# Kernel optimization log

Hardware: AMD Instinct MI355X
Metric: run time of the kernel (lower is better)

The kernel has to match this reference:

```python
import jax, jax.numpy as jnp
import numpy as np

NUM_GROUPS = 32
EPS = 1e-6
NUM_HEADS = 8


def group_norm32(x, gamma, beta):
    # GroupNorm32: compute in float32, cast back to input dtype.
    b, c, h, w = x.shape
    xf = x.astype(jnp.float32).reshape(b, NUM_GROUPS, -1)  # [b, G, (C/G)*h*w]
    mean = xf.mean(axis=-1, keepdims=True)
    var = xf.var(axis=-1, keepdims=True)
    xn = ((xf - mean) * jax.lax.rsqrt(var + EPS)).reshape(b, c, h, w)
    xn = xn * gamma[None, :, None, None] + beta[None, :, None, None]
    return xn.astype(x.dtype)


def setup_inputs() -> dict:
    key = jax.random.key(0)
    ks = jax.random.split(key, 4)
    b, c, h, w = 16, 512, 32, 32
    x = jax.random.normal(ks[0], (b, c, h, w), dtype=jnp.float32)
    w_qkv = jax.random.normal(ks[1], (3 * c, c), dtype=jnp.float32) * (1.0 / np.sqrt(c))
    b_qkv = jnp.zeros((3 * c,), dtype=jnp.float32)
    w_proj = jax.random.normal(ks[2], (c, c), dtype=jnp.float32) * (1.0 / np.sqrt(c))
    b_proj = jnp.zeros((c,), dtype=jnp.float32)
    gamma = jnp.ones((c,), dtype=jnp.float32)
    beta = jnp.zeros((c,), dtype=jnp.float32)
    return {"x": x, "w_qkv": w_qkv, "b_qkv": b_qkv, "w_proj": w_proj,
            "b_proj": b_proj, "gamma": gamma, "beta": beta}


def reference(x, w_qkv, b_qkv, w_proj, b_proj, gamma, beta):
    b, c, h, w = x.shape
    H = NUM_HEADS
    d = c // H
    n = h * w
    x_norm = group_norm32(x, gamma, beta)
    # 1x1 conv == channel matmul
    qkv = jnp.einsum('oc,bchw->bohw', w_qkv, x_norm) + b_qkv[None, :, None, None]
    q, k, v = jnp.split(qkv, 3, axis=1)
    q = q.reshape(b, H, d, n)
    k = k.reshape(b, H, d, n)
    v = v.reshape(b, H, d, n)
    scale = d ** (-0.5)
    attn = jnp.einsum('bhdn,bhdm->bhnm', q, k) * scale  # [b,H,n,n]
    attn = jax.nn.softmax(attn, axis=-1)
    out = jnp.einsum('bhnm,bhdm->bhdn', attn, v).reshape(b, c, h, w)
    proj = jnp.einsum('oc,bchw->bohw', w_proj, out) + b_proj[None, :, None, None]
    return x + proj
```

## Files before the change

### kernel.cpp

```cpp
#include <hip/hip_runtime.h>
#include <hip/hip_bf16.h>

typedef __bf16 bf16;
typedef __bf16 bf16x4 __attribute__((ext_vector_type(4)));
typedef __bf16 bf16x8 __attribute__((ext_vector_type(8)));
typedef float  floatx4 __attribute__((ext_vector_type(4)));
typedef float  f32x16  __attribute__((ext_vector_type(16)));

#define BB   16
#define CC   512
#define NN   1024
#define GG   32
#define CPG  16
#define HH   8
#define DD   64
#define QSCALE 0.18033688011f

#if __has_builtin(__builtin_amdgcn_exp2f)
#define EXP2(x) __builtin_amdgcn_exp2f(x)
#else
#define EXP2(x) exp2f(x)
#endif

__device__ inline floatx4 mfma16(bf16x8 a, bf16x8 b, floatx4 c) {
    return __builtin_amdgcn_mfma_f32_16x16x32_bf16(a, b, c, 0, 0, 0);
}
__device__ inline f32x16 mfma32(bf16x8 a, bf16x8 b, f32x16 c) {
    return __builtin_amdgcn_mfma_f32_32x32x16_bf16(a, b, c, 0, 0, 0);
}

__device__ inline floatx4 zero4() {
    floatx4 z; z[0] = 0.f; z[1] = 0.f; z[2] = 0.f; z[3] = 0.f; return z;
}

__device__ inline void gl_lds16(const bf16* g, bf16* l) {
    __builtin_amdgcn_global_load_lds(
        (const __attribute__((address_space(1))) unsigned int*)g,
        (__attribute__((address_space(3))) unsigned int*)l, 16, 0, 0);
}

__device__ inline unsigned cvt_pk_bf16(float a, float b) {
    unsigned r;
    asm("v_cvt_pk_bf16_f32 %0, %1, %2" : "=v"(r) : "v"(a), "v"(b));
    return r;
}
__device__ inline void pl32swap(unsigned &x, unsigned &y) {
    asm volatile("v_permlane32_swap_b32 %0, %1" : "+v"(x), "+v"(y));
}

__device__ inline float ldf(const void* p, size_t i, int isb) {
    return isb ? (float)((const bf16*)p)[i] : ((const float*)p)[i];
}
__device__ inline floatx4 ldf4(const void* p, size_t i, int isb) {
    floatx4 o;
    if (isb) {
        bf16x4 v = *(const bf16x4*)((const bf16*)p + i);
        #pragma unroll
        for (int j = 0; j < 4; ++j) o[j] = (float)v[j];
    } else {
        o = *(const floatx4*)((const float*)p + i);
    }
    return o;
}
__device__ inline void stf(void* p, size_t i, float v, int isb) {
    if (isb) ((bf16*)p)[i] = (bf16)v; else ((float*)p)[i] = v;
}

__global__ __launch_bounds__(256) void flag_kernel(const void* x, const void* wq,
        const void* wp, const void* gamma, int* flags) {
    __shared__ int bad[3];
    const int tid = threadIdx.x;
    if (tid < 3) bad[tid] = 0;
    __syncthreads();
    const void* arrs[3] = {x, wq, wp};
    #pragma unroll
    for (int a = 0; a < 3; ++a) {
        const unsigned short* u = (const unsigned short*)arrs[a];
        int c = 0;
        for (int i = tid * 32; i < tid * 32 + 32; ++i) {
            if ((u[i] & 0x7F80) == 0x7F80) c = 1;
        }
        if (c) atomicOr(&bad[a], 1);
    }
    __syncthreads();
    if (tid == 0) {
        flags[0] = bad[0] ? 0 : 1;
        flags[1] = bad[1] ? 0 : 1;
        flags[2] = bad[2] ? 0 : 1;
        flags[3] = (((const unsigned short*)gamma)[0] == 0x3F80) ? 1 : 0;
    }
}

__global__ __launch_bounds__(256) void cvt2_kernel(const void* __restrict__ src1,
        const void* __restrict__ src2, bf16* __restrict__ dst1,
        bf16* __restrict__ dst2, const int* __restrict__ flags) {
    const int NQKV = 3 * CC * CC;
    int i = (blockIdx.x * 256 + threadIdx.x) * 4;
    const void* src; bf16* dst; int f;
    if (i < NQKV) {
        src = src1; dst = dst1; f = flags[1];
    } else {
        src = src2; dst = dst2; f = flags[2]; i -= NQKV;
    }
    if (f) {
        *(bf16x4*)(dst + i) = *(const bf16x4*)((const bf16*)src + i);
    } else {
        const float* s = (const float*)src + i;
        bf16x4 o;
        #pragma unroll
        for (int j = 0; j < 4; ++j) o[j] = (bf16)s[j];
        *(bf16x4*)(dst + i) = o;
    }
}

__global__ __launch_bounds__(256) void gn_kernel(const void* __restrict__ x,
        const void* __restrict__ gamma, const void* __restrict__ beta,
        bf16* __restrict__ xn_t, const int* __restrict__ flags, int b0) {
    const int fx = flags[0], fg = flags[3];
    const int bg = blockIdx.x;
    const int bl = bg >> 5, g = bg & 31;
    const int tid = threadIdx.x;
    const size_t xbase = (size_t)((b0 + bl) * CC + g * CPG) * NN;

    float s = 0.f, ss = 0.f;
    for (int i = tid * 4; i < CPG * NN; i += 1024) {
        floatx4 v = ldf4(x, xbase + i, fx);
        #pragma unroll
        for (int j = 0; j < 4; ++j) { s += v[j]; ss += v[j] * v[j]; }
    }
    for (int off = 32; off > 0; off >>= 1) {
        s  += __shfl_down(s, off);
        ss += __shfl_down(ss, off);
    }
    __shared__ float red[8];
    __shared__ float stats[2];
    const int wave = tid >> 6;
    if ((tid & 63) == 0) { red[wave] = s; red[4 + wave] = ss; }
    __syncthreads();
    if (tid == 0) {
        float S  = red[0] + red[1] + red[2] + red[3];
        float SS = red[4] + red[5] + red[6] + red[7];
        float mean = S * (1.0f / (CPG * NN));
        float var  = SS * (1.0f / (CPG * NN)) - mean * mean;
        stats[0] = mean;
        stats[1] = rsqrtf(fmaxf(var, 0.f) + 1e-6f);
    }
    __syncthreads();
    const float mean = stats[0], rstd = stats[1];

    __shared__ __align__(16) float tile[4][CPG][66];
    const int l = tid & 63;
    const int cn = l >> 2;
    const int nb = (l & 3) * 16;
    const float gm1 = ldf(gamma, g * CPG + cn, fg);
    const float bt1 = ldf(beta,  g * CPG + cn, fg);
    const int n2 = l >> 2, cq = l & 3;
    float (*tw)[66] = tile[wave];

    for (int nt = wave; nt < NN / 64; nt += 4) {
        #pragma unroll
        for (int k = 0; k < 4; ++k) {
            floatx4 v = ldf4(x, xbase + (size_t)cn * NN + nt * 64 + nb + k * 4, fx);
            #pragma unroll
            for (int j = 0; j < 4; ++j)
                tw[cn][nb + k * 4 + j] = (v[j] - mean) * rstd * gm1 + bt1;
        }
        asm volatile("s_waitcnt lgkmcnt(0)" ::: "memory");
        #pragma unroll
        for (int m = 0; m < 4; ++m) {
            const int n2m = n2 + m * 16;
            bf16x4 o;
            #pragma unroll
            for (int k = 0; k < 4; ++k) o[k] = (bf16)tw[cq * 4 + k][n2m];
            *(bf16x4*)(xn_t + (size_t)(bl * NN + nt * 64 + n2m) * CC + g * CPG + cq * 4) = o;
        }
        asm volatile("s_waitcnt lgkmcnt(0)" ::: "memory");
    }
}

__global__ __launch_bounds__(256) void qkv_kernel(const bf16* __restrict__ wq_b,
        const bf16* __restrict__ b_qkv, const bf16* __restrict__ xn_t,
        bf16* __restrict__ q_t, bf16* __restrict__ k_pk, bf16* __restrict__ v_pk) {
    __shared__ __align__(16) bf16 As[2][128 * 32];
    __shared__ __align__(16) bf16 Bs[2][128 * 32];

    const int ntile = blockIdx.x;
    const int mtile = blockIdx.y;
    const int bl = blockIdx.z;
    const int w = threadIdx.x >> 6, lane = threadIdx.x & 63;
    const int l16 = lane & 15, quad = lane >> 4;
    const int wr = w >> 1, wc = w & 1;

    const int mbase = mtile * 128, nbase = ntile * 128;
    const int srow = lane >> 2;
    const int scol = (((lane & 3) ^ ((srow >> 1) & 3)) << 3);
    const bf16* Ag = wq_b + (size_t)(mbase + w * 32 + srow) * CC + scol;
    const bf16* Bg = xn_t + (size_t)bl * NN * CC + (size_t)(nbase + w * 32 + srow) * CC + scol;
    const int ldso = (2 * w) * 512;

#define QSTAGE(buf, k0) do {                                  \
    gl_lds16(Ag + (k0),           &As[buf][ldso]);            \
    gl_lds16(Ag + 16 * CC + (k0), &As[buf][ldso + 512]);      \
    gl_lds16(Bg + (k0),           &Bs[buf][ldso]);            \
    gl_lds16(Bg + 16 * CC + (k0), &Bs[buf][ldso + 512]);      \
} while (0)

    floatx4 acc[4][4];
    #pragma unroll
    for (int i = 0; i < 4; ++i)
        #pragma unroll
        for (int j = 0; j < 4; ++j) acc[i][j] = zero4();

    const int sw = (l16 >> 1) & 3;
    QSTAGE(0, 0);

    for (int it = 0; it < 16; ++it) {
        const int cur = it & 1;
        const int nk = ((it + 1) & 15) * 32;
        QSTAGE(cur ^ 1, nk);
        asm volatile("s_waitcnt vmcnt(4)" ::: "memory");
        __builtin_amdgcn_s_barrier();

        bf16x8 af[4], bfr[4];
        #pragma unroll
        for (int mt = 0; mt < 4; ++mt)
            af[mt] = *(const bf16x8*)&As[cur][(wr * 64 + mt * 16 + l16) * 32 + ((quad ^ sw) << 3)];
        #pragma unroll
        for (int nt = 0; nt < 4; ++nt)
            bfr[nt] = *(const bf16x8*)&Bs[cur][(wc * 64 + nt * 16 + l16) * 32 + ((quad ^ sw) << 3)];

        asm volatile("s_waitcnt lgkmcnt(0)" ::: "memory");
        __builtin_amdgcn_s_barrier();

        #pragma unroll
        for (int mt = 0; mt < 4; ++mt)
            #pragma unroll
            for (int nt = 0; nt < 4; ++nt)
                acc[mt][nt] = mfma16(af[mt], bfr[nt], acc[mt][nt]);
    }
#undef QSTAGE

    const int qsel = mtile >> 2;
    const int obase = (mtile & 3) * 128;
    #pragma unroll
    for (int mt = 0; mt < 4; ++mt) {
        const int op = obase + wr * 64 + mt * 16 + quad * 4;
        float bias[4];
        #pragma unroll
        for (int r = 0; r < 4; ++r) bias[r] = (float)b_qkv[qsel * CC + op + r];
        #pragma unroll
        for (int nt = 0; nt < 4; ++nt) {
            const int p = nbase + wc * 64 + nt * 16 + l16;
            if (qsel == 0) {
                int h = op >> 6, d0 = op & 63;
                bf16x4 o;
                #pragma unroll
                for (int r = 0; r < 4; ++r) o[r] = (bf16)((acc[mt][nt][r] + bias[r]) * QSCALE);
                *(bf16x4*)(q_t + ((size_t)(bl * HH + h) * NN + p) * DD + d0) = o;
            } else if (qsel == 1) {
                int h = op >> 6, d0 = op & 63;
                bf16x4 o;
                #pragma unroll
                for (int r = 0; r < 4; ++r) o[r] = (bf16)(acc[mt][nt][r] + bias[r]);
                size_t off = ((size_t)(bl * HH + h) << 16) + ((size_t)(p >> 5) << 11)
                           + ((d0 >> 4) << 9) + (((d0 >> 3) & 1) << 8)
                           + ((p & 31) << 3) + (d0 & 7);
                *(bf16x4*)(k_pk + off) = o;
            } else {
                #pragma unroll
                for (int r = 0; r < 4; ++r) {
                    int c = op + r;
                    int h = c >> 6, d = c & 63;
                    size_t off = ((size_t)(bl * HH + h) << 16) + ((size_t)(p >> 4) << 10)
                               + ((d >> 5) << 9) + (((p >> 3) & 1) << 8)
                               + ((d & 31) << 3) + (p & 7);
                    v_pk[off] = (bf16)(acc[mt][nt][r] + bias[r]);
                }
            }
        }
    }
}

__global__ __launch_bounds__(256) void attn_kernel(const bf16* __restrict__ q_t,
        const bf16* __restrict__ k_pk, const bf16* __restrict__ v_pk,
        bf16* __restrict__ attn_out) {
    const int lid = blockIdx.x + (blockIdx.y << 2);
    const int xcd = lid & 7, jj = lid >> 3;
    const int bh = xcd * (gridDim.y >> 3) + (jj >> 2);
    const int qb = jj & 3;
    const int bl = bh >> 3, h = bh & 7;
    const int tid = threadIdx.x;
    const int w = tid >> 6, lane = tid & 63;
    const int l31 = lane & 31, hi = lane >> 5;

    const bf16* kpb = k_pk + ((size_t)bh << 16) + (hi << 8) + (l31 << 3);
    const bf16* vpb = v_pk + ((size_t)bh << 16) + (hi << 8) + (l31 << 3);

    const int qbase = qb * 256 + w * 64;
    const bf16* qp = q_t + ((size_t)bh * NN + qbase + l31) * DD + hi * 8;
    bf16x8 qf0[4], qf1[4];
    #pragma unroll
    for (int ks = 0; ks < 4; ++ks) {
        qf0[ks] = *(const bf16x8*)(qp + ks * 16);
        qf1[ks] = *(const bf16x8*)(qp + (size_t)32 * DD + ks * 16);
    }

    f32x16 oacc0[2], oacc1[2];
    #pragma unroll
    for (int i = 0; i < 2; ++i)
        #pragma unroll
        for (int r = 0; r < 16; ++r) { oacc0[i][r] = 0.f; oacc1[i][r] = 0.f; }
    float lrun0 = 0.f, lrun1 = 0.f;

#define EXPPACK(SV, PW, LR) do {                                          \
    float p[16];                                                          \
    _Pragma("unroll")                                                     \
    for (int r = 0; r < 16; ++r) { p[r] = EXP2((SV)[r]); LR += p[r]; }    \
    _Pragma("unroll")                                                     \
    for (int i = 0; i < 8; ++i) PW[i] = cvt_pk_bf16(p[2*i], p[2*i+1]);    \
    pl32swap(PW[0], PW[2]); pl32swap(PW[1], PW[3]);                       \
    pl32swap(PW[4], PW[6]); pl32swap(PW[5], PW[7]);                       \
} while (0)

    bf16x8 kf[4];
    #pragma unroll
    for (int ks = 0; ks < 4; ++ks)
        kf[ks] = *(const bf16x8*)(kpb + (ks << 9));

    #pragma unroll 2
    for (int kb = 0; kb < 32; ++kb) {
        bf16x8 vfr[4];
        #pragma unroll
        for (int tt = 0; tt < 2; ++tt)
            #pragma unroll
            for (int db = 0; db < 2; ++db)
                vfr[tt * 2 + db] = *(const bf16x8*)(vpb + (size_t)((kb * 2 + tt) << 10) + (db << 9));
        const int kbn = (kb + 1) & 31;
        bf16x8 kfn[4];
        #pragma unroll
        for (int ks = 0; ks < 4; ++ks)
            kfn[ks] = *(const bf16x8*)(kpb + (size_t)(kbn << 11) + (ks << 9));

        f32x16 s0, s1;
        #pragma unroll
        for (int r = 0; r < 16; ++r) { s0[r] = 0.f; s1[r] = 0.f; }
        #pragma unroll
        for (int ks = 0; ks < 4; ++ks) s0 = mfma32(kf[ks], qf0[ks], s0);
        #pragma unroll
        for (int ks = 0; ks < 4; ++ks) s1 = mfma32(kf[ks], qf1[ks], s1);

        unsigned pw0[8], pw1[8];
        EXPPACK(s0, pw0, lrun0);
        EXPPACK(s1, pw1, lrun1);

        #pragma unroll
        for (int tt = 0; tt < 2; ++tt) {
            union { unsigned u[4]; bf16x8 v; } pf0, pf1;
            #pragma unroll
            for (int i = 0; i < 4; ++i) {
                pf0.u[i] = pw0[tt * 4 + i];
                pf1.u[i] = pw1[tt * 4 + i];
            }
            #pragma unroll
            for (int db = 0; db < 2; ++db) {
                bf16x8 vf = vfr[tt * 2 + db];
                oacc0[db] = mfma32(vf, pf0.v, oacc0[db]);
                oacc1[db] = mfma32(vf, pf1.v, oacc1[db]);
            }
        }
        #pragma unroll
        for (int ks = 0; ks < 4; ++ks) kf[ks] = kfn[ks];
    }
#undef EXPPACK

    lrun0 += __shfl_xor(lrun0, 32);
    lrun1 += __shfl_xor(lrun1, 32);
    const float inv0 = 1.0f / lrun0;
    const float inv1 = 1.0f / lrun1;
    bf16* ob0 = attn_out + ((size_t)bl * NN + qbase + l31) * CC + h * DD;
    bf16* ob1 = ob0 + (size_t)32 * CC;
    #pragma unroll
    for (int db = 0; db < 2; ++db) {
        #pragma unroll
        for (int g = 0; g < 4; ++g) {
            bf16x4 o0, o1;
            #pragma unroll
            for (int e = 0; e < 4; ++e) {
                o0[e] = (bf16)(oacc0[db][4 * g + e] * inv0);
                o1[e] = (bf16)(oacc1[db][4 * g + e] * inv1);
            }
            *(bf16x4*)(ob0 + db * 32 + g * 8 + hi * 4) = o0;
            *(bf16x4*)(ob1 + db * 32 + g * 8 + hi * 4) = o1;
        }
    }
}

__global__ __launch_bounds__(256) void proj_kernel(const bf16* __restrict__ wp_b,
        const bf16* __restrict__ b_proj, const bf16* __restrict__ attn_out,
        const void* __restrict__ x, void* __restrict__ out,
        const int* __restrict__ flags, int b0) {
    __shared__ __align__(16) bf16 As[2][128 * 32];
    __shared__ __align__(16) bf16 Bs[2][128 * 32];

    const int fx = flags[0];
    const int ntile = blockIdx.x;
    const int mtile = blockIdx.y;
    const int bl = blockIdx.z;
    const int w = threadIdx.x >> 6, lane = threadIdx.x & 63;
    const int l16 = lane & 15, quad = lane >> 4;
    const int wr = w >> 1, wc = w & 1;

    const int mbase = mtile * 128, nbase = ntile * 128;
    const int srow = lane >> 2;
    const int scol = (((lane & 3) ^ ((srow >> 1) & 3)) << 3);
    const bf16* Ag = wp_b + (size_t)(mbase + w * 32 + srow) * CC + scol;
    const bf16* Bg = attn_out + (size_t)bl * NN * CC + (size_t)(nbase + w * 32 + srow) * CC + scol;
    const int ldso = (2 * w) * 512;

#define PSTAGE(buf, k0) do {                                  \
    gl_lds16(Ag + (k0),           &As[buf][ldso]);            \
    gl_lds16(Ag + 16 * CC + (k0), &As[buf][ldso + 512]);      \
    gl_lds16(Bg + (k0),           &Bs[buf][ldso]);            \
    gl_lds16(Bg + 16 * CC + (k0), &Bs[buf][ldso + 512]);      \
} while (0)

    floatx4 acc[4][4];
    #pragma unroll
    for (int i = 0; i < 4; ++i)
        #pragma unroll
        for (int j = 0; j < 4; ++j) acc[i][j] = zero4();

    const int sw = (l16 >> 1) & 3;
    PSTAGE(0, 0);

    for (int it = 0; it < 16; ++it) {
        const int cur = it & 1;
        const int nk = ((it + 1) & 15) * 32;
        PSTAGE(cur ^ 1, nk);
        asm volatile("s_waitcnt vmcnt(4)" ::: "memory");
        __builtin_amdgcn_s_barrier();

        bf16x8 af[4], bfr[4];
        #pragma unroll
        for (int mt = 0; mt < 4; ++mt)
            af[mt] = *(const bf16x8*)&As[cur][(wr * 64 + mt * 16 + l16) * 32 + ((quad ^ sw) << 3)];
        #pragma unroll
        for (int nt = 0; nt < 4; ++nt)
            bfr[nt] = *(const bf16x8*)&Bs[cur][(wc * 64 + nt * 16 + l16) * 32 + ((quad ^ sw) << 3)];

        asm volatile("s_waitcnt lgkmcnt(0)" ::: "memory");
        __builtin_amdgcn_s_barrier();

        #pragma unroll
        for (int mt = 0; mt < 4; ++mt)
            #pragma unroll
            for (int nt = 0; nt < 4; ++nt)
                acc[mt][nt] = mfma16(af[mt], bfr[nt], acc[mt][nt]);
    }
#undef PSTAGE

    #pragma unroll
    for (int mt = 0; mt < 4; ++mt) {
        const int op = mbase + wr * 64 + mt * 16 + quad * 4;
        float bias[4];
        #pragma unroll
        for (int r = 0; r < 4; ++r) bias[r] = (float)b_proj[op + r];
        #pragma unroll
        for (int nt = 0; nt < 4; ++nt) {
            const int p = nbase + wc * 64 + nt * 16 + l16;
            #pragma unroll
            for (int r = 0; r < 4; ++r) {
                size_t idx = ((size_t)(b0 + bl) * CC + op + r) * NN + p;
                float xv = ldf(x, idx, fx);
                stf(out, idx, xv + acc[mt][nt][r] + bias[r], fx);
            }
        }
    }
}

extern "C" void kernel_launch(void* const* d_in, const int* in_sizes, int n_in,
                              void* d_out, int out_size, void* d_ws, size_t ws_size,
                              hipStream_t stream) {
    const void* x      = d_in[0];
    const void* w_qkv  = d_in[1];
    const bf16* b_qkv  = (const bf16*)d_in[2];
    const void* w_proj = d_in[3];
    const bf16* b_proj = (const bf16*)d_in[4];
    const void* gamma  = d_in[5];
    const void* beta   = d_in[6];

    const size_t MB = (size_t)1 << 20;
    const int NQKV = 3 * CC * CC;
    const int NPRJ = CC * CC;
    const size_t wbytes = (size_t)(NQKV + NPRJ) * sizeof(bf16) + 4096;
    int bc = 0;
    for (int c = 16; c >= 1; c >>= 1) {
        if ((size_t)c * 4 * MB + wbytes <= ws_size) { bc = c; break; }
    }
    if (bc == 0) {
        hipMemsetAsync(d_out, 0, (size_t)out_size * sizeof(bf16), stream);
        return;
    }

    const size_t cs = (size_t)bc * MB;
    char* ws = (char*)d_ws;
    bf16* xn_t = (bf16*)(ws);
    bf16* q_t  = (bf16*)(ws + cs);
    bf16* k_pk = (bf16*)(ws + 2 * cs);
    bf16* v_pk = (bf16*)(ws + 3 * cs);
    int*  flags = (int*)(ws + 4 * cs);
    bf16* wq_b = (bf16*)(ws + 4 * cs + 4096);
    bf16* wp_b = wq_b + NQKV;
    bf16* attn_out = xn_t;

    flag_kernel<<<1, 256, 0, stream>>>(x, w_qkv, w_proj, gamma, flags);
    cvt2_kernel<<<(NQKV + NPRJ) / 1024, 256, 0, stream>>>(w_qkv, w_proj, wq_b, wp_b, flags);

    for (int b0 = 0; b0 < BB; b0 += bc) {
        gn_kernel<<<dim3(bc * GG), 256, 0, stream>>>(x, gamma, beta, xn_t, flags, b0);
        qkv_kernel<<<dim3(8, 12, bc), 256, 0, stream>>>(wq_b, b_qkv, xn_t, q_t, k_pk, v_pk);
        attn_kernel<<<dim3(4, bc * HH), 256, 0, stream>>>(q_t, k_pk, v_pk, attn_out);
        proj_kernel<<<dim3(8, 4, bc), 256, 0, stream>>>(wp_b, b_proj, attn_out, x, d_out, flags, b0);
    }
}
```

Baseline: 231.3 us.

## Enlarge QKV GEMM tiles to 256x256x64 with 8 waves and staged prefetch

Reworks the QKV projection GEMM so each 512-thread block computes a 256x256 output tile with K-steps of 64, where previously 256-thread blocks computed 128x128 tiles with K-steps of 32. Global-to-LDS prefetch of the next stage is split into four quarters interleaved with the MFMA sub-phases, and s_setprio raises wave priority around the MFMA bursts. The aim is more operand reuse per LDS load and fewer barriers per FLOP. In exchange the grid shrinks to 24 blocks per batch, LDS use grows to 128 KB per block, and register pressure rises, which may lower occupancy and leave CUs underused at small batch chunks.

```diff
diff --git a/kernel.cpp b/kernel.cpp
--- a/kernel.cpp
+++ b/kernel.cpp
@@ -178,103 +178,155 @@
     }
 }
 
-__global__ __launch_bounds__(256) void qkv_kernel(const bf16* __restrict__ wq_b,
+__global__ __launch_bounds__(512) void qkv_kernel(const bf16* __restrict__ wq_b,
         const bf16* __restrict__ b_qkv, const bf16* __restrict__ xn_t,
         bf16* __restrict__ q_t, bf16* __restrict__ k_pk, bf16* __restrict__ v_pk) {
-    __shared__ __align__(16) bf16 As[2][128 * 32];
-    __shared__ __align__(16) bf16 Bs[2][128 * 32];
+    __shared__ __align__(16) bf16 As[2][256 * 64];
+    __shared__ __align__(16) bf16 Bs[2][256 * 64];
 
     const int ntile = blockIdx.x;
     const int mtile = blockIdx.y;
     const int bl = blockIdx.z;
     const int w = threadIdx.x >> 6, lane = threadIdx.x & 63;
     const int l16 = lane & 15, quad = lane >> 4;
-    const int wr = w >> 1, wc = w & 1;
-
-    const int mbase = mtile * 128, nbase = ntile * 128;
-    const int srow = lane >> 2;
-    const int scol = (((lane & 3) ^ ((srow >> 1) & 3)) << 3);
-    const bf16* Ag = wq_b + (size_t)(mbase + w * 32 + srow) * CC + scol;
-    const bf16* Bg = xn_t + (size_t)bl * NN * CC + (size_t)(nbase + w * 32 + srow) * CC + scol;
-    const int ldso = (2 * w) * 512;
-
-#define QSTAGE(buf, k0) do {                                  \
-    gl_lds16(Ag + (k0),           &As[buf][ldso]);            \
-    gl_lds16(Ag + 16 * CC + (k0), &As[buf][ldso + 512]);      \
-    gl_lds16(Bg + (k0),           &Bs[buf][ldso]);            \
-    gl_lds16(Bg + 16 * CC + (k0), &Bs[buf][ldso + 512]);      \
+    const int wr = w >> 2, wc = w & 3;
+
+    const int mbase = mtile * 256, nbase = ntile * 256;
+
+    const int srow8 = lane >> 3;
+    const int schunk = (lane & 7) ^ ((w * 2 + (lane >> 5)) & 3);
+    const bf16* Ag = wq_b + (size_t)(mbase + w * 8 + srow8) * CC + schunk * 8;
+    const bf16* Bg = xn_t + (size_t)bl * NN * CC
+                   + (size_t)(nbase + w * 8 + srow8) * CC + schunk * 8;
+    const int ldsb = (w * 8) * 64;
+
+#define STG(buf, k0, q) do {                                                        \
+    gl_lds16(Ag + (size_t)((q) * 64) * CC + (k0), &As[buf][(q) * 4096 + ldsb]);     \
+    gl_lds16(Bg + (size_t)((q) * 64) * CC + (k0), &Bs[buf][(q) * 4096 + ldsb]);     \
 } while (0)
 
-    floatx4 acc[4][4];
-    #pragma unroll
-    for (int i = 0; i < 4; ++i)
+    floatx4 acc[8][4];
+    #pragma unroll
+    for (int i = 0; i < 8; ++i)
         #pragma unroll
         for (int j = 0; j < 4; ++j) acc[i][j] = zero4();
 
-    const int sw = (l16 >> 1) & 3;
-    QSTAGE(0, 0);
-
-    for (int it = 0; it < 16; ++it) {
-        const int cur = it & 1;
-        const int nk = ((it + 1) & 15) * 32;
-        QSTAGE(cur ^ 1, nk);
-        asm volatile("s_waitcnt vmcnt(4)" ::: "memory");
-        __builtin_amdgcn_s_barrier();
-
-        bf16x8 af[4], bfr[4];
-        #pragma unroll
-        for (int mt = 0; mt < 4; ++mt)
-            af[mt] = *(const bf16x8*)&As[cur][(wr * 64 + mt * 16 + l16) * 32 + ((quad ^ sw) << 3)];
+    const int swz = (l16 >> 2) & 3;
+
+    STG(0, 0, 0); STG(0, 0, 1); STG(0, 0, 2); STG(0, 0, 3);
+
+    for (int t = 0; t < 8; ++t) {
+        const int cur = t & 1, nxt = cur ^ 1;
+        const int k0n = (t + 1) * 64;
+        const bool pf = (t < 7);
+
+        if (pf) {
+            STG(nxt, k0n, 0);
+            asm volatile("s_waitcnt vmcnt(2)" ::: "memory");
+        } else {
+            asm volatile("s_waitcnt vmcnt(0)" ::: "memory");
+        }
+        __builtin_amdgcn_s_barrier();
+
+        bf16x8 bfr[4], af[4];
         #pragma unroll
         for (int nt = 0; nt < 4; ++nt)
-            bfr[nt] = *(const bf16x8*)&Bs[cur][(wc * 64 + nt * 16 + l16) * 32 + ((quad ^ sw) << 3)];
-
-        asm volatile("s_waitcnt lgkmcnt(0)" ::: "memory");
-        __builtin_amdgcn_s_barrier();
-
+            bfr[nt] = *(const bf16x8*)&Bs[cur][(wc * 64 + nt * 16 + l16) * 64 + ((quad ^ swz) << 3)];
+        #pragma unroll
+        for (int mt = 0; mt < 4; ++mt)
+            af[mt] = *(const bf16x8*)&As[cur][(wr * 128 + mt * 16 + l16) * 64 + ((quad ^ swz) << 3)];
+        asm volatile("s_waitcnt lgkmcnt(0)" ::: "memory");
+        __builtin_amdgcn_s_barrier();
+        __builtin_amdgcn_s_setprio(1);
         #pragma unroll
         for (int mt = 0; mt < 4; ++mt)
             #pragma unroll
             for (int nt = 0; nt < 4; ++nt)
                 acc[mt][nt] = mfma16(af[mt], bfr[nt], acc[mt][nt]);
-    }
-#undef QSTAGE
-
-    const int qsel = mtile >> 2;
-    const int obase = (mtile & 3) * 128;
-    #pragma unroll
-    for (int mt = 0; mt < 4; ++mt) {
-        const int op = obase + wr * 64 + mt * 16 + quad * 4;
+        __builtin_amdgcn_s_setprio(0);
+
+        #pragma unroll
+        for (int mt = 0; mt < 4; ++mt)
+            af[mt] = *(const bf16x8*)&As[cur][(wr * 128 + 64 + mt * 16 + l16) * 64 + ((quad ^ swz) << 3)];
+        if (pf) STG(nxt, k0n, 1);
+        asm volatile("s_waitcnt lgkmcnt(0)" ::: "memory");
+        __builtin_amdgcn_s_barrier();
+        __builtin_amdgcn_s_setprio(1);
+        #pragma unroll
+        for (int mt = 0; mt < 4; ++mt)
+            #pragma unroll
+            for (int nt = 0; nt < 4; ++nt)
+                acc[4 + mt][nt] = mfma16(af[mt], bfr[nt], acc[4 + mt][nt]);
+        __builtin_amdgcn_s_setprio(0);
+
+        #pragma unroll
+        for (int nt = 0; nt < 4; ++nt)
+            bfr[nt] = *(const bf16x8*)&Bs[cur][(wc * 64 + nt * 16 + l16) * 64 + (((4 + quad) ^ swz) << 3)];
+        #pragma unroll
+        for (int mt = 0; mt < 4; ++mt)
+            af[mt] = *(const bf16x8*)&As[cur][(wr * 128 + mt * 16 + l16) * 64 + (((4 + quad) ^ swz) << 3)];
+        if (pf) STG(nxt, k0n, 2);
+        asm volatile("s_waitcnt lgkmcnt(0)" ::: "memory");
+        __builtin_amdgcn_s_barrier();
+        __builtin_amdgcn_s_setprio(1);
+        #pragma unroll
+        for (int mt = 0; mt < 4; ++mt)
+            #pragma unroll
+            for (int nt = 0; nt < 4; ++nt)
+                acc[mt][nt] = mfma16(af[mt], bfr[nt], acc[mt][nt]);
+        __builtin_amdgcn_s_setprio(0);
+
+        #pragma unroll
+        for (int mt = 0; mt < 4; ++mt)
+            af[mt] = *(const bf16x8*)&As[cur][(wr * 128 + 64 + mt * 16 + l16) * 64 + (((4 + quad) ^ swz) << 3)];
+        if (pf) STG(nxt, k0n, 3);
+        asm volatile("s_waitcnt lgkmcnt(0)" ::: "memory");
+        __builtin_amdgcn_s_barrier();
+        __builtin_amdgcn_s_setprio(1);
+        #pragma unroll
+        for (int mt = 0; mt < 4; ++mt)
+            #pragma unroll
+            for (int nt = 0; nt < 4; ++nt)
+                acc[4 + mt][nt] = mfma16(af[mt], bfr[nt], acc[4 + mt][nt]);
+        __builtin_amdgcn_s_setprio(0);
+    }
+#undef STG
+
+    #pragma unroll
+    for (int r8 = 0; r8 < 8; ++r8) {
+        const int op = mbase + wr * 128 + r8 * 16 + quad * 4;
+        const int qsel = op >> 9;
+        const int opq  = op & 511;
         float bias[4];
         #pragma unroll
-        for (int r = 0; r < 4; ++r) bias[r] = (float)b_qkv[qsel * CC + op + r];
+        for (int rr = 0; rr < 4; ++rr) bias[rr] = (float)b_qkv[qsel * CC + opq + rr];
         #pragma unroll
         for (int nt = 0; nt < 4; ++nt) {
             const int p = nbase + wc * 64 + nt * 16 + l16;
             if (qsel == 0) {
-                int h = op >> 6, d0 = op & 63;
+                int h = opq >> 6, d0 = opq & 63;
                 bf16x4 o;
                 #pragma unroll
-                for (int r = 0; r < 4; ++r) o[r] = (bf16)((acc[mt][nt][r] + bias[r]) * QSCALE);
+                for (int rr = 0; rr < 4; ++rr) o[rr] = (bf16)((acc[r8][nt][rr] + bias[rr]) * QSCALE);
                 *(bf16x4*)(q_t + ((size_t)(bl * HH + h) * NN + p) * DD + d0) = o;
             } else if (qsel == 1) {
-                int h = op >> 6, d0 = op & 63;
+                int h = opq >> 6, d0 = opq & 63;
                 bf16x4 o;
                 #pragma unroll
-                for (int r = 0; r < 4; ++r) o[r] = (bf16)(acc[mt][nt][r] + bias[r]);
+                for (int rr = 0; rr < 4; ++rr) o[rr] = (bf16)(acc[r8][nt][rr] + bias[rr]);
                 size_t off = ((size_t)(bl * HH + h) << 16) + ((size_t)(p >> 5) << 11)
                            + ((d0 >> 4) << 9) + (((d0 >> 3) & 1) << 8)
                            + ((p & 31) << 3) + (d0 & 7);
                 *(bf16x4*)(k_pk + off) = o;
             } else {
                 #pragma unroll
-                for (int r = 0; r < 4; ++r) {
-                    int c = op + r;
+                for (int rr = 0; rr < 4; ++rr) {
+                    int c = opq + rr;
                     int h = c >> 6, d = c & 63;
                     size_t off = ((size_t)(bl * HH + h) << 16) + ((size_t)(p >> 4) << 10)
                                + ((d >> 5) << 9) + (((p >> 3) & 1) << 8)
                                + ((d & 31) << 3) + (p & 7);
-                    v_pk[off] = (bf16)(acc[mt][nt][r] + bias[r]);
+                    v_pk[off] = (bf16)(acc[r8][nt][rr] + bias[rr]);
                 }
             }
         }
@@ -518,7 +570,7 @@
 
     for (int b0 = 0; b0 < BB; b0 += bc) {
         gn_kernel<<<dim3(bc * GG), 256, 0, stream>>>(x, gamma, beta, xn_t, flags, b0);
-        qkv_kernel<<<dim3(8, 12, bc), 256, 0, stream>>>(wq_b, b_qkv, xn_t, q_t, k_pk, v_pk);
+        qkv_kernel<<<dim3(4, 6, bc), 512, 0, stream>>>(wq_b, b_qkv, xn_t, q_t, k_pk, v_pk);
         attn_kernel<<<dim3(4, bc * HH), 256, 0, stream>>>(q_t, k_pk, v_pk, attn_out);
         proj_kernel<<<dim3(8, 4, bc), 256, 0, stream>>>(wp_b, b_proj, attn_out, x, d_out, flags, b0);
     }
```

Measured after the change: 239.7 us. 3.6% more time.
